# Optimization experiments

Measured on AMD Instinct MI355X. Metric: run time of the kernel, lower is better.

Reference implementation:

```python
import jax, jax.numpy as jnp
import numpy as np

N = 131072          # batch of (action, condition) pairs
ACT_D = 12          # action_dim
COND_D = 256        # condition_dim
K = 256             # num_embeddings (codebook size)
E = 16              # embedding_dim
H1, H2 = 512, 256   # encoder_hidden_dims
COMMIT = 0.25       # commitment_cost
EPS_NORM = 1e-12    # F.normalize eps


def _normalize(x):
    n = jnp.linalg.norm(x, axis=-1, keepdims=True)
    return x / jnp.maximum(n, EPS_NORM)


def setup_inputs() -> dict:
    key = jax.random.key(0)
    ks = jax.random.split(key, 16)
    s = 0.02
    return {
        "actions": jax.random.normal(ks[0], (N, ACT_D), jnp.float32),
        "conditions": jax.random.normal(ks[1], (N, COND_D), jnp.float32),
        # encoder: (COND_D+ACT_D) -> H1 -> H2 -> E  (weights stored [in, out])
        "enc_w1": jax.random.normal(ks[2], (COND_D + ACT_D, H1), jnp.float32) * s,
        "enc_b1": jnp.zeros((H1,), jnp.float32),
        "enc_w2": jax.random.normal(ks[3], (H1, H2), jnp.float32) * s,
        "enc_b2": jnp.zeros((H2,), jnp.float32),
        "enc_w3": jax.random.normal(ks[4], (H2, E), jnp.float32) * s,
        "enc_b3": jnp.zeros((E,), jnp.float32),
        # decoder: (COND_D+E) -> H2 -> H1 -> ACT_D
        "dec_w1": jax.random.normal(ks[5], (COND_D + E, H2), jnp.float32) * s,
        "dec_b1": jnp.zeros((H2,), jnp.float32),
        "dec_w2": jax.random.normal(ks[6], (H2, H1), jnp.float32) * s,
        "dec_b2": jnp.zeros((H1,), jnp.float32),
        "dec_w3": jax.random.normal(ks[7], (H1, ACT_D), jnp.float32) * s,
        "dec_b3": jnp.zeros((ACT_D,), jnp.float32),
        # codebook, init U(-1/K, 1/K) like nn.Embedding in the module
        "embedding": jax.random.uniform(ks[8], (K, E), jnp.float32, -1.0 / K, 1.0 / K),
    }


def reference(actions, conditions, enc_w1, enc_b1, enc_w2, enc_b2, enc_w3, enc_b3,
              dec_w1, dec_b1, dec_w2, dec_b2, dec_w3, dec_b3, embedding):
    sg = jax.lax.stop_gradient
    elu = jax.nn.elu

    # ---- encoder ----
    x = jnp.concatenate([actions, conditions], axis=-1)          # [N, ACT_D+COND_D]
    h = elu(x @ enc_w1 + enc_b1)
    h = elu(h @ enc_w2 + enc_b2)
    z = h @ enc_w3 + enc_b3                                      # [N, E]

    # ---- vector quantizer (distance='cos') ----
    normed_in = sg(_normalize(z))                                # inputs.detach()
    normed_w = _normalize(embedding)
    distances = normed_in @ normed_w.T                           # [N, K] cosine sims

    idx = jnp.argmax(distances, axis=-1)                         # [N]
    quantized = embedding[idx]                                   # one-hot @ codebook == gather

    e_latent_loss = COMMIT * jnp.mean((sg(quantized) - z) ** 2)
    q_latent_loss = jnp.mean((quantized - sg(z)) ** 2)
    quantized_st = z + sg(quantized - z)                         # straight-through

    counts = jnp.zeros((K,), distances.dtype).at[idx].add(1.0)
    avg_probs = counts / N                                       # mean of one-hot encodings
    perplexity = jnp.exp(-jnp.sum(avg_probs * jnp.log(avg_probs + 1e-10)))

    # ---- contrastive loss (training branch, deterministic part) ----
    sortd = jnp.sort(distances, axis=0)                          # ascending per codeword
    n_pos = max(1, N // K)
    dis_pos = jnp.mean(sortd[-n_pos:, :], axis=0, keepdims=True) # [1, K] hardest positives
    dis_neg = sortd[: N // 2, :]                                 # [N//2, K]
    dis = jnp.concatenate([dis_pos, dis_neg], axis=0).T / 0.07   # [K, 1+N//2]
    # cross-entropy with target class 0
    contra_loss = jnp.mean(jax.nn.logsumexp(dis, axis=1) - dis[:, 0])

    # ---- decoder ----
    d = jnp.concatenate([quantized_st, conditions], axis=-1)     # [N, E+COND_D]
    d = elu(d @ dec_w1 + dec_b1)
    d = elu(d @ dec_w2 + dec_b2)
    reconstructed = d @ dec_w3 + dec_b3                          # [N, ACT_D]

    reconstruction_loss = jnp.mean((reconstructed - actions) ** 2)

    return (reconstructed, quantized_st, idx.astype(jnp.int32), q_latent_loss,
            e_latent_loss, contra_loss, perplexity, reconstruction_loss)
```

## Files before the change

### kernel.cpp

```cpp
#include <hip/hip_runtime.h>
#include <hip/hip_bf16.h>
#include <math.h>

#define NROWS 131072
#define ACT_D 12
#define COND_D 256
#define KEMB 256
#define EDIM 16
#define H1D 512
#define H2D 256
#define NB 16384

typedef __attribute__((ext_vector_type(8))) _Float16 half8;
typedef __attribute__((ext_vector_type(4))) float floatx4;
typedef unsigned short ushort_t;

#define LO_SCALE 4096.0f
#define INV_LO_SCALE 2.44140625e-4f


__global__ void init_kernel(int* counts, float* outScal) {
    int t = threadIdx.x;
    counts[t] = 0;
    if (t < 5) outScal[t] = 0.0f;
}

__device__ inline ushort_t f16bits(_Float16 h) { return __builtin_bit_cast(ushort_t, h); }
__device__ inline float f16pair(ushort_t a, ushort_t b) {
    return (float)__builtin_bit_cast(_Float16, a)
         + (float)__builtin_bit_cast(_Float16, b) * INV_LO_SCALE;
}
__device__ inline void splitf(float v, ushort_t& hi, ushort_t& lo) {
    _Float16 h = (_Float16)v;
    _Float16 l = (_Float16)((v - (float)h) * LO_SCALE);
    hi = f16bits(h); lo = f16bits(l);
}

__device__ inline void gload_lds16(const void* g, void* lds) {
    __builtin_amdgcn_global_load_lds((const __attribute__((address_space(1))) void*)g,
                                     (__attribute__((address_space(3))) void*)lds, 16, 0, 0);
}

__global__ __launch_bounds__(256)
void convw_kernel(const float* __restrict__ W, ushort_t* __restrict__ Whi,
                  ushort_t* __restrict__ Wlo, int K, int N, int Kp)
{
    int n = blockIdx.x;
    int k = blockIdx.y * 256 + threadIdx.x;
    if (k >= Kp) return;
    float v = (k < K) ? W[(long)k * N + n] : 0.0f;
    ushort_t h, l; splitf(v, h, l);
    Whi[(long)n * Kp + k] = h;
    Wlo[(long)n * Kp + k] = l;
}

template<int CONCAT>
__global__ __launch_bounds__(256, 3)
void gemm_f16x3_kernel(const void* A0v, const void* A1v,
                       const ushort_t* __restrict__ Bhi, const ushort_t* __restrict__ Blo,
                       const float* __restrict__ bias,
                       ushort_t* __restrict__ Chi, ushort_t* __restrict__ Clo,
                       int Nw, int Kp, int Kvalid)
{
    __shared__ uint lds[12288];
    const int tid = threadIdx.x;
    const int w = tid >> 6, l = tid & 63;
    const int quad = l >> 4, lr = l & 15;
    const long rowBase = (long)blockIdx.x * 64;
    const int colBase = blockIdx.y * 128;
    const int nQ = w * 32;

    floatx4 accH[4][2], accX[4][2];
#pragma unroll
    for (int i = 0; i < 4; ++i)
#pragma unroll
        for (int j = 0; j < 2; ++j) { accH[i][j] = (floatx4)(0.0f); accX[i][j] = (floatx4)(0.0f); }

    auto stage = [&](int buf, int k0) {
        const int base = buf * 6144;
#pragma unroll
        for (int h = 0; h < 2; ++h) {
            const ushort_t* g = Bhi + (long)(colBase + h * 64 + l) * Kp + k0 + w * 8;
            gload_lds16(g, &lds[base + 2048 + w * 512 + h * 256]);
        }
#pragma unroll
        for (int h = 0; h < 2; ++h) {
            const ushort_t* g = Blo + (long)(colBase + h * 64 + l) * Kp + k0 + w * 8;
            gload_lds16(g, &lds[base + 4096 + w * 512 + h * 256]);
        }
        if (CONCAT == 0) {
            const ushort_t* gh = (const ushort_t*)A0v + (rowBase + l) * Kp + k0 + w * 8;
            gload_lds16(gh, &lds[base + w * 256]);
            const ushort_t* gl = (const ushort_t*)A1v + (rowBase + l) * Kp + k0 + w * 8;
            gload_lds16(gl, &lds[base + 1024 + w * 256]);
        } else {
            const float* A1 = (const float*)A0v;
            const float* A2 = (const float*)A1v;
            const long grow = rowBase + l;
            const int kk = k0 + w * 8;
            float v[8];
            if (kk >= CONCAT && kk + 8 <= Kvalid) {
                const float* p = A2 + grow * COND_D + (kk - CONCAT);
                *(float4*)&v[0] = *(const float4*)p;
                *(float4*)&v[4] = *(const float4*)(p + 4);
            } else if (kk + 8 <= CONCAT) {
                const float* p = A1 + grow * CONCAT + kk;
                *(float4*)&v[0] = *(const float4*)p;
                *(float4*)&v[4] = *(const float4*)(p + 4);
            } else {
#pragma unroll
                for (int i = 0; i < 8; ++i) {
                    int k = kk + i;
                    v[i] = (k < CONCAT) ? A1[grow * CONCAT + k]
                         : (k < Kvalid) ? A2[grow * COND_D + (k - CONCAT)] : 0.0f;
                }
            }
            uint hh[4], ll[4];
#pragma unroll
            for (int i = 0; i < 4; ++i) {
                ushort_t h0, l0, h1, l1;
                splitf(v[2 * i], h0, l0);
                splitf(v[2 * i + 1], h1, l1);
                hh[i] = (uint)h0 | ((uint)h1 << 16);
                ll[i] = (uint)l0 | ((uint)l1 << 16);
            }
            *(uint4*)&lds[base + w * 256 + l * 4]        = *(uint4*)hh;
            *(uint4*)&lds[base + 1024 + w * 256 + l * 4] = *(uint4*)ll;
        }
    };

    auto compute = [&](int buf) {
        const int base = buf * 6144;
        half8 bh[2], bl[2];
#pragma unroll
        for (int jn = 0; jn < 2; ++jn) {
            int boff = base + 2048 + quad * 512 + (nQ + jn * 16 + lr) * 4;
            bh[jn] = __builtin_bit_cast(half8, *(uint4*)&lds[boff]);
            bl[jn] = __builtin_bit_cast(half8, *(uint4*)&lds[boff + 2048]);
        }
#pragma unroll
        for (int im = 0; im < 4; ++im) {
            int aoff = base + quad * 256 + (im * 16 + lr) * 4;
            half8 ah = __builtin_bit_cast(half8, *(uint4*)&lds[aoff]);
            half8 al = __builtin_bit_cast(half8, *(uint4*)&lds[aoff + 1024]);
#pragma unroll
            for (int jn = 0; jn < 2; ++jn) {
                accH[im][jn] = __builtin_amdgcn_mfma_f32_16x16x32_f16(ah, bh[jn], accH[im][jn], 0, 0, 0);
                accX[im][jn] = __builtin_amdgcn_mfma_f32_16x16x32_f16(ah, bl[jn], accX[im][jn], 0, 0, 0);
                accX[im][jn] = __builtin_amdgcn_mfma_f32_16x16x32_f16(al, bh[jn], accX[im][jn], 0, 0, 0);
            }
        }
    };

    const int kTiles = Kp / 32;
    stage(0, 0);
    __syncthreads();
    int cur = 0;
    for (int t = 0; t < kTiles - 1; ++t) {
        stage(cur ^ 1, (t + 1) * 32);
        compute(cur);
        __syncthreads();
        cur ^= 1;
    }
    compute(cur);

    float bv[2];
#pragma unroll
    for (int jn = 0; jn < 2; ++jn) bv[jn] = bias[colBase + nQ + jn * 16 + lr];
#pragma unroll
    for (int im = 0; im < 4; ++im) {
#pragma unroll
        for (int jn = 0; jn < 2; ++jn) {
            int n = colBase + nQ + jn * 16 + lr;
#pragma unroll
            for (int rr = 0; rr < 4; ++rr) {
                long m = rowBase + im * 16 + quad * 4 + rr;
                float x = accH[im][jn][rr] + accX[im][jn][rr] * INV_LO_SCALE + bv[jn];
                x = x > 0.0f ? x : (expf(x) - 1.0f);
                ushort_t h, lo; splitf(x, h, lo);
                long idx = m * Nw + n;
                Chi[idx] = h;
                Clo[idx] = lo;
            }
        }
    }
}

__global__ __launch_bounds__(256)
void quantize_kernel(const ushort_t* __restrict__ h2hi, const ushort_t* __restrict__ h2lo,
                     const float* __restrict__ W3,
                     const float* __restrict__ b3, const float* __restrict__ emb,
                     float* __restrict__ distT, float* __restrict__ outQ,
                     float* __restrict__ outIdx, int* __restrict__ counts,
                     float* __restrict__ qsum)
{
    __shared__ float h2t[16 * 260];
    __shared__ float w3t[16 * 260];
    __shared__ float nwt[256 * 20];
    __shared__ float zt[16 * 17];
    __shared__ float dt[16 * 257];
    __shared__ int   lcnt[256];
    __shared__ float swred[4];

    int t = threadIdx.x;
    long rowBase = (long)blockIdx.x * 16;

    for (int it = 0; it < 16; ++it) {
        long idx = (rowBase + it) * 256 + t;
        h2t[it * 260 + t] = f16pair(h2hi[idx], h2lo[idx]);
    }
    for (int it = 0; it < 16; ++it) {
        int flat = it * 256 + t;
        int j = flat >> 4, c = flat & 15;
        w3t[c * 260 + j] = W3[flat];
    }
    {
        float e0[16]; float ss = 0.f;
#pragma unroll
        for (int i = 0; i < 16; ++i) { e0[i] = emb[t * 16 + i]; ss += e0[i] * e0[i]; }
        float inv = 1.0f / fmaxf(sqrtf(ss), 1e-12f);
#pragma unroll
        for (int i = 0; i < 16; ++i) nwt[t * 20 + i] = e0[i] * inv;
    }
    lcnt[t] = 0;
    __syncthreads();

    int r = t >> 4, c = t & 15;
    float zacc = b3[c];
    for (int j4 = 0; j4 < 64; ++j4) {
        float4 h = *(const float4*)&h2t[r * 260 + j4 * 4];
        float4 w = *(const float4*)&w3t[c * 260 + j4 * 4];
        zacc += h.x * w.x + h.y * w.y + h.z * w.z + h.w * w.w;
    }
    float ss = zacc * zacc;
#pragma unroll
    for (int m = 1; m < 16; m <<= 1) ss += __shfl_xor(ss, m, 64);
    zt[r * 17 + c] = zacc / fmaxf(sqrtf(ss), 1e-12f);
    __syncthreads();

    float zr[16];
#pragma unroll
    for (int e = 0; e < 16; ++e) zr[e] = zt[r * 17 + e];
    float best = -1e30f; int bidx = 0;
    for (int cc = 0; cc < 16; ++cc) {
        int col = cc * 16 + c;
        float d = 0.f;
#pragma unroll
        for (int e4 = 0; e4 < 4; ++e4) {
            float4 wv = *(const float4*)&nwt[col * 20 + e4 * 4];
            d += zr[e4 * 4 + 0] * wv.x + zr[e4 * 4 + 1] * wv.y
               + zr[e4 * 4 + 2] * wv.z + zr[e4 * 4 + 3] * wv.w;
        }
        dt[r * 257 + col] = d;
        if (d > best || (d == best && col < bidx)) { best = d; bidx = col; }
    }
#pragma unroll
    for (int m = 1; m < 16; m <<= 1) {
        float ov = __shfl_xor(best, m, 64);
        int   oi = __shfl_xor(bidx, m, 64);
        if (ov > best || (ov == best && oi < bidx)) { best = ov; bidx = oi; }
    }

    float q = emb[bidx * 16 + c];
    outQ[(rowBase + r) * 16 + c] = q;
    float df = q - zacc;
    float part = df * df;
#pragma unroll
    for (int m = 1; m < 64; m <<= 1) part += __shfl_xor(part, m, 64);
    if ((t & 63) == 0) swred[t >> 6] = part;
    if (c == 0) {
        outIdx[rowBase + r] = (float)bidx;
        atomicAdd(&lcnt[bidx], 1);
    }
    __syncthreads();
    if (t == 0) atomicAdd(qsum, swred[0] + swred[1] + swred[2] + swred[3]);
    if (lcnt[t] > 0) atomicAdd(&counts[t], lcnt[t]);

    int rr = t & 15, cg = t >> 4;
    for (int i = 0; i < 16; ++i) {
        int col = i * 16 + cg;
        distT[(long)col * NROWS + rowBase + rr] = dt[rr * 257 + col];
    }
}

__global__ __launch_bounds__(1024)
void selA_kernel(const float* __restrict__ distT, int* __restrict__ stats)
{
    __shared__ int hist[NB];
    __shared__ int part[1024];
    int t = threadIdx.x, c = blockIdx.x;
    for (int i = t; i < NB; i += 1024) hist[i] = 0;
    __syncthreads();
    const float* col = distT + (long)c * NROWS;
    for (int i = t; i < NROWS; i += 1024) {
        float v = col[i];
        int b = (int)((v + 1.0f) * (NB * 0.5f));
        b = min(max(b, 0), NB - 1);
        atomicAdd(&hist[b], 1);
    }
    __syncthreads();
    const int CH = NB / 1024;
    int s = 0;
    for (int i = 0; i < CH; ++i) s += hist[t * CH + i];
    part[t] = s;
    __syncthreads();
    if (t == 0) {
        int target = NROWS / 2;
        int cum = 0; int chunk = 0;
        while (cum + part[chunk] < target) { cum += part[chunk]; ++chunk; }
        int b = chunk * CH;
        while (cum + hist[b] < target) { cum += hist[b]; ++b; }
        int medBin = b, needLow = target - cum, cntMed = hist[b];
        int cumA = 0; chunk = 1023;
        while (cumA + part[chunk] < 512) { cumA += part[chunk]; --chunk; }
        b = chunk * CH + CH - 1;
        while (cumA + hist[b] < 512) { cumA += hist[b]; --b; }
        int topBin = b, needTop = 512 - cumA, cntTop = hist[b];
        int* st = stats + c * 6;
        st[0] = medBin; st[1] = needLow; st[2] = cntMed;
        st[3] = topBin; st[4] = needTop; st[5] = cntTop;
    }
}

__global__ __launch_bounds__(1024)
void selB_kernel(const float* __restrict__ distT, const int* __restrict__ stats,
                 float* __restrict__ contra_sum)
{
    __shared__ float red[64];
    int t = threadIdx.x, c = blockIdx.x;
    const int* st = stats + c * 6;
    int medBin = st[0], needLow = st[1], cntMed = st[2];
    int topBin = st[3], needTop = st[4], cntTop = st[5];
    const float binw = 2.0f / NB;
    float mUp = -1.0f + (medBin + 1) * binw;
    const float INVT = 1.0f / 0.07f;
    const float* col = distT + (long)c * NROWS;
    float topS = 0.f, tbS = 0.f, lowS = 0.f, mbS = 0.f;
    for (int i = t; i < NROWS; i += 1024) {
        float v = col[i];
        int b = (int)((v + 1.0f) * (NB * 0.5f));
        b = min(max(b, 0), NB - 1);
        if (b > topBin)       topS += v;
        else if (b == topBin) tbS += v;
        if (b < medBin)       lowS += expf((v - mUp) * INVT);
        else if (b == medBin) mbS  += expf((v - mUp) * INVT);
    }
#pragma unroll
    for (int m = 1; m < 64; m <<= 1) {
        topS += __shfl_xor(topS, m, 64);
        tbS  += __shfl_xor(tbS, m, 64);
        lowS += __shfl_xor(lowS, m, 64);
        mbS  += __shfl_xor(mbS, m, 64);
    }
    if ((t & 63) == 0) {
        int wv = t >> 6;
        red[wv * 4 + 0] = topS; red[wv * 4 + 1] = tbS;
        red[wv * 4 + 2] = lowS; red[wv * 4 + 3] = mbS;
    }
    __syncthreads();
    if (t == 0) {
        float T0 = 0, T1 = 0, T2 = 0, T3 = 0;
        for (int wv = 0; wv < 16; ++wv) {
            T0 += red[wv * 4 + 0]; T1 += red[wv * 4 + 1];
            T2 += red[wv * 4 + 2]; T3 += red[wv * 4 + 3];
        }
        float dis_pos = (T0 + needTop * (T1 / cntTop)) * (1.0f / 512.0f);
        float S = T2 + needLow * (T3 / cntMed);
        float colContra = log1pf(S * expf((mUp - dis_pos) * INVT));
        atomicAdd(contra_sum, colContra);
    }
}

__global__ __launch_bounds__(256)
void dec3_kernel(const ushort_t* __restrict__ d2hi, const ushort_t* __restrict__ d2lo,
                 const float* __restrict__ W,
                 const float* __restrict__ bias, const float* __restrict__ actions,
                 float* __restrict__ rec, float* __restrict__ recon_sum)
{
    __shared__ float dtile[16 * 516];
    __shared__ float wt[512 * 12];
    __shared__ float red2[4];
    int t = threadIdx.x;
    long rowBase = (long)blockIdx.x * 16;
    for (int it = 0; it < 24; ++it) wt[it * 256 + t] = W[it * 256 + t];
    for (int it = 0; it < 32; ++it) {
        int flat = it * 256 + t;
        int r = flat >> 9, k = flat & 511;
        long idx = (rowBase + r) * 512 + k;
        dtile[r * 516 + k] = f16pair(d2hi[idx], d2lo[idx]);
    }
    __syncthreads();
    float part = 0.f;
    if (t < 192) {
        int r = t / 12, cc = t % 12;
        float acc = bias[cc];
        for (int k4 = 0; k4 < 128; ++k4) {
            float4 h = *(const float4*)&dtile[r * 516 + k4 * 4];
            acc += h.x * wt[(k4 * 4 + 0) * 12 + cc] + h.y * wt[(k4 * 4 + 1) * 12 + cc]
                 + h.z * wt[(k4 * 4 + 2) * 12 + cc] + h.w * wt[(k4 * 4 + 3) * 12 + cc];
        }
        rec[(rowBase + r) * 12 + cc] = acc;
        float df = acc - actions[(rowBase + r) * 12 + cc];
        part = df * df;
    }
#pragma unroll
    for (int m = 1; m < 64; m <<= 1) part += __shfl_xor(part, m, 64);
    if ((t & 63) == 0) red2[t >> 6] = part;
    __syncthreads();
    if (t == 0) atomicAdd(recon_sum, red2[0] + red2[1] + red2[2] + red2[3]);
}

__global__ void finalize_kernel(const int* __restrict__ counts, float* __restrict__ outScal)
{
    __shared__ float red[4];
    int t = threadIdx.x;
    float p = counts[t] * (1.0f / NROWS);
    float term = p * logf(p + 1e-10f);
#pragma unroll
    for (int m = 1; m < 64; m <<= 1) term += __shfl_xor(term, m, 64);
    if ((t & 63) == 0) red[t >> 6] = term;
    __syncthreads();
    if (t == 0) {
        float hsum = red[0] + red[1] + red[2] + red[3];
        float qsum = outScal[0], contra = outScal[2], recon = outScal[4];
        float ql = qsum * (1.0f / (NROWS * 16.0f));
        outScal[0] = ql;
        outScal[1] = 0.25f * ql;
        outScal[2] = contra * (1.0f / 256.0f);
        outScal[3] = expf(-hsum);
        outScal[4] = recon * (1.0f / (NROWS * 12.0f));
    }
}

extern "C" void kernel_launch(void* const* d_in, const int* in_sizes, int n_in,
                              void* d_out, int out_size, void* d_ws, size_t ws_size,
                              hipStream_t stream)
{
    const float* actions    = (const float*)d_in[0];
    const float* conditions = (const float*)d_in[1];
    const float* enc_w1 = (const float*)d_in[2];
    const float* enc_b1 = (const float*)d_in[3];
    const float* enc_w2 = (const float*)d_in[4];
    const float* enc_b2 = (const float*)d_in[5];
    const float* enc_w3 = (const float*)d_in[6];
    const float* enc_b3 = (const float*)d_in[7];
    const float* dec_w1 = (const float*)d_in[8];
    const float* dec_b1 = (const float*)d_in[9];
    const float* dec_w2 = (const float*)d_in[10];
    const float* dec_b2 = (const float*)d_in[11];
    const float* dec_w3 = (const float*)d_in[12];
    const float* dec_b3 = (const float*)d_in[13];
    const float* emb    = (const float*)d_in[14];

    float* out     = (float*)d_out;
    float* outRec  = out;
    float* outQ    = out + (long)NROWS * 12;
    float* outIdx  = out + (long)NROWS * 28;
    float* outScal = out + (long)NROWS * 29;

    ushort_t* wb    = (ushort_t*)d_out;
    ushort_t* w1hi  = wb;            ushort_t* w1lo  = wb + 147456;
    ushort_t* w2hi  = wb + 294912;   ushort_t* w2lo  = wb + 425984;
    ushort_t* wd1hi = wb + 557056;   ushort_t* wd1lo = wb + 630784;
    ushort_t* wd2hi = wb + 704512;   ushort_t* wd2lo = wb + 835584;

    float* ws = (float*)d_ws;
    int* counts = (int*)ws;
    int* stats  = (int*)(ws + 256);
    ushort_t* h2hi = (ushort_t*)(ws + 1792);
    ushort_t* h2lo = (ushort_t*)(ws + 16779008);
    ushort_t* d1hi = h2hi;
    ushort_t* d1lo = h2lo;
    float*    P1   = ws + 33556224;
    ushort_t* h1hi = (ushort_t*)P1;
    ushort_t* h1lo = (ushort_t*)(ws + 67110656);
    float*    distT = P1;
    ushort_t* d2hi = h1hi;
    ushort_t* d2lo = h1lo;

    hipLaunchKernelGGL(init_kernel, dim3(1), dim3(256), 0, stream, counts, outScal);
    hipLaunchKernelGGL(convw_kernel, dim3(512, 2), dim3(256), 0, stream, enc_w1, w1hi, w1lo, 268, 512, 288);
    hipLaunchKernelGGL(convw_kernel, dim3(256, 2), dim3(256), 0, stream, enc_w2, w2hi, w2lo, 512, 256, 512);
    hipLaunchKernelGGL(convw_kernel, dim3(256, 2), dim3(256), 0, stream, dec_w1, wd1hi, wd1lo, 272, 256, 288);
    hipLaunchKernelGGL(convw_kernel, dim3(512, 1), dim3(256), 0, stream, dec_w2, wd2hi, wd2lo, 256, 512, 256);
    hipLaunchKernelGGL((gemm_f16x3_kernel<ACT_D>), dim3(2048, 4), dim3(256), 0, stream,
                       (const void*)actions, (const void*)conditions, w1hi, w1lo, enc_b1,
                       h1hi, h1lo, H1D, 288, 268);
    hipLaunchKernelGGL((gemm_f16x3_kernel<0>), dim3(2048, 2), dim3(256), 0, stream,
                       (const void*)h1hi, (const void*)h1lo, w2hi, w2lo, enc_b2,
                       h2hi, h2lo, H2D, 512, 512);
    hipLaunchKernelGGL(quantize_kernel, dim3(8192), dim3(256), 0, stream,
                       h2hi, h2lo, enc_w3, enc_b3, emb, distT, outQ, outIdx, counts, &outScal[0]);
    hipLaunchKernelGGL(selA_kernel, dim3(256), dim3(1024), 0, stream, distT, stats);
    hipLaunchKernelGGL(selB_kernel, dim3(256), dim3(1024), 0, stream, distT, stats, &outScal[2]);
    hipLaunchKernelGGL((gemm_f16x3_kernel<EDIM>), dim3(2048, 2), dim3(256), 0, stream,
                       (const void*)outQ, (const void*)conditions, wd1hi, wd1lo, dec_b1,
                       d1hi, d1lo, H2D, 288, 272);
    hipLaunchKernelGGL((gemm_f16x3_kernel<0>), dim3(2048, 4), dim3(256), 0, stream,
                       (const void*)d1hi, (const void*)d1lo, wd2hi, wd2lo, dec_b2,
                       d2hi, d2lo, H1D, 256, 256);
    hipLaunchKernelGGL(dec3_kernel, dim3(8192), dim3(256), 0, stream,
                       d2hi, d2lo, dec_w3, dec_b3, actions, outRec, &outScal[4]);
    hipLaunchKernelGGL(finalize_kernel, dim3(1), dim3(256), 0, stream, counts, outScal);
}
```

Measured before the change: 1.566 ms.

## Pipeline GEMM staging with explicit vmcnt waits and split barriers

Restructures the double-buffered GEMM main loop so global-to-LDS loads for the next tile stay in flight across compute. It uses partial s_waitcnt vmcnt counts and raw s_barrier in place of a full __syncthreads. For the concat path, the fp32 A loads are issued early into registers and split/written to LDS after compute, which hides their latency. It also raises wave priority during MFMA compute and hoists pointer arithmetic out of the loop. The hand-tuned waitcnt counts are fragile: if they do not match the actual number of outstanding loads, the result can be silently wrong.

```diff
diff --git a/kernel.cpp b/kernel.cpp
--- a/kernel.cpp
+++ b/kernel.cpp
@@ -76,57 +76,65 @@
 #pragma unroll
         for (int j = 0; j < 2; ++j) { accH[i][j] = (floatx4)(0.0f); accX[i][j] = (floatx4)(0.0f); }
 
-    auto stage = [&](int buf, int k0) {
-        const int base = buf * 6144;
-#pragma unroll
-        for (int h = 0; h < 2; ++h) {
-            const ushort_t* g = Bhi + (long)(colBase + h * 64 + l) * Kp + k0 + w * 8;
-            gload_lds16(g, &lds[base + 2048 + w * 512 + h * 256]);
-        }
-#pragma unroll
-        for (int h = 0; h < 2; ++h) {
-            const ushort_t* g = Blo + (long)(colBase + h * 64 + l) * Kp + k0 + w * 8;
-            gload_lds16(g, &lds[base + 4096 + w * 512 + h * 256]);
-        }
-        if (CONCAT == 0) {
-            const ushort_t* gh = (const ushort_t*)A0v + (rowBase + l) * Kp + k0 + w * 8;
-            gload_lds16(gh, &lds[base + w * 256]);
-            const ushort_t* gl = (const ushort_t*)A1v + (rowBase + l) * Kp + k0 + w * 8;
-            gload_lds16(gl, &lds[base + 1024 + w * 256]);
+    const ushort_t* pBh0 = Bhi + (long)(colBase + l) * Kp + w * 8;
+    const ushort_t* pBh1 = pBh0 + (long)64 * Kp;
+    const ushort_t* pBl0 = Blo + (long)(colBase + l) * Kp + w * 8;
+    const ushort_t* pBl1 = pBl0 + (long)64 * Kp;
+
+    auto stageB = [&](int buf, int k0) {
+        uint* d = &lds[buf * 6144 + 2048 + w * 512];
+        gload_lds16(pBh0 + k0, d);
+        gload_lds16(pBh1 + k0, d + 256);
+        gload_lds16(pBl0 + k0, d + 2048);
+        gload_lds16(pBl1 + k0, d + 2048 + 256);
+    };
+
+    const ushort_t* pAh = (const ushort_t*)A0v + (rowBase + l) * Kp + w * 8;
+    const ushort_t* pAl = (const ushort_t*)A1v + (rowBase + l) * Kp + w * 8;
+    auto stageA0 = [&](int buf, int k0) {
+        uint* d = &lds[buf * 6144 + w * 256];
+        gload_lds16(pAh + k0, d);
+        gload_lds16(pAl + k0, d + 1024);
+    };
+
+    const float* A1p = (const float*)A0v;
+    const float* A2p = (const float*)A1v;
+    const long grow = rowBase + l;
+
+    auto aload = [&](float* v, int k0) -> bool {
+        const int kk = k0 + w * 8;
+        if (kk >= CONCAT && kk + 8 <= Kvalid) {
+            const float* p = A2p + grow * COND_D + (kk - CONCAT);
+            *(float4*)&v[0] = *(const float4*)p;
+            *(float4*)&v[4] = *(const float4*)(p + 4);
+            return true;
+        } else if (kk + 8 <= CONCAT) {
+            const float* p = A1p + grow * CONCAT + kk;
+            *(float4*)&v[0] = *(const float4*)p;
+            *(float4*)&v[4] = *(const float4*)(p + 4);
+            return true;
         } else {
-            const float* A1 = (const float*)A0v;
-            const float* A2 = (const float*)A1v;
-            const long grow = rowBase + l;
-            const int kk = k0 + w * 8;
-            float v[8];
-            if (kk >= CONCAT && kk + 8 <= Kvalid) {
-                const float* p = A2 + grow * COND_D + (kk - CONCAT);
-                *(float4*)&v[0] = *(const float4*)p;
-                *(float4*)&v[4] = *(const float4*)(p + 4);
-            } else if (kk + 8 <= CONCAT) {
-                const float* p = A1 + grow * CONCAT + kk;
-                *(float4*)&v[0] = *(const float4*)p;
-                *(float4*)&v[4] = *(const float4*)(p + 4);
-            } else {
-#pragma unroll
-                for (int i = 0; i < 8; ++i) {
-                    int k = kk + i;
-                    v[i] = (k < CONCAT) ? A1[grow * CONCAT + k]
-                         : (k < Kvalid) ? A2[grow * COND_D + (k - CONCAT)] : 0.0f;
-                }
+#pragma unroll
+            for (int i = 0; i < 8; ++i) {
+                int k = kk + i;
+                v[i] = (k < CONCAT) ? A1p[grow * CONCAT + k]
+                     : (k < Kvalid) ? A2p[grow * COND_D + (k - CONCAT)] : 0.0f;
             }
-            uint hh[4], ll[4];
-#pragma unroll
-            for (int i = 0; i < 4; ++i) {
-                ushort_t h0, l0, h1, l1;
-                splitf(v[2 * i], h0, l0);
-                splitf(v[2 * i + 1], h1, l1);
-                hh[i] = (uint)h0 | ((uint)h1 << 16);
-                ll[i] = (uint)l0 | ((uint)l1 << 16);
-            }
-            *(uint4*)&lds[base + w * 256 + l * 4]        = *(uint4*)hh;
-            *(uint4*)&lds[base + 1024 + w * 256 + l * 4] = *(uint4*)ll;
-        }
+            return false;
+        }
+    };
+    auto awrite = [&](int buf, const float* v) {
+        uint hh[4], ll[4];
+#pragma unroll
+        for (int i = 0; i < 4; ++i) {
+            ushort_t h0, l0, h1, l1;
+            splitf(v[2 * i], h0, l0);
+            splitf(v[2 * i + 1], h1, l1);
+            hh[i] = (uint)h0 | ((uint)h1 << 16);
+            ll[i] = (uint)l0 | ((uint)l1 << 16);
+        }
+        *(uint4*)&lds[buf * 6144 + w * 256 + l * 4]        = *(uint4*)hh;
+        *(uint4*)&lds[buf * 6144 + 1024 + w * 256 + l * 4] = *(uint4*)ll;
     };
 
     auto compute = [&](int buf) {
@@ -153,15 +161,51 @@
     };
 
     const int kTiles = Kp / 32;
-    stage(0, 0);
-    __syncthreads();
     int cur = 0;
+    float v[8];
+    bool fast = true;
+    (void)fast;
+
+    if constexpr (CONCAT == 0) {
+        stageB(0, 0);
+        stageA0(0, 0);
+    } else {
+        fast = aload(v, 0);
+        stageB(0, 0);
+        awrite(0, v);
+        asm volatile("s_waitcnt lgkmcnt(0)" ::: "memory");
+        __builtin_amdgcn_sched_barrier(0);
+    }
+
     for (int t = 0; t < kTiles - 1; ++t) {
-        stage(cur ^ 1, (t + 1) * 32);
+        const int k0n = (t + 1) * 32;
+        if constexpr (CONCAT == 0) {
+            stageB(cur ^ 1, k0n);
+            stageA0(cur ^ 1, k0n);
+            asm volatile("s_waitcnt vmcnt(6)" ::: "memory");
+            __builtin_amdgcn_sched_barrier(0);
+        } else {
+            fast = aload(v, k0n);
+            stageB(cur ^ 1, k0n);
+            if (fast) asm volatile("s_waitcnt vmcnt(6)" ::: "memory");
+            else      asm volatile("s_waitcnt vmcnt(4)" ::: "memory");
+            __builtin_amdgcn_sched_barrier(0);
+        }
+        __builtin_amdgcn_s_barrier();
+        __builtin_amdgcn_s_setprio(1);
         compute(cur);
-        __syncthreads();
+        __builtin_amdgcn_s_setprio(0);
+        if constexpr (CONCAT != 0) {
+            awrite(cur ^ 1, v);
+            asm volatile("s_waitcnt lgkmcnt(0)" ::: "memory");
+            __builtin_amdgcn_sched_barrier(0);
+        }
+        __builtin_amdgcn_s_barrier();
         cur ^= 1;
     }
+    asm volatile("s_waitcnt vmcnt(0)" ::: "memory");
+    __builtin_amdgcn_sched_barrier(0);
+    __builtin_amdgcn_s_barrier();
     compute(cur);
 
     float bv[2];
```

New measurement: 1.583 ms. About the same (+1.1%).
